# Kernel tuning notes

Hardware: AMD Instinct MI355X
Metric: run time of the kernel (lower is better)

Reference implementation:

```python
import jax, jax.numpy as jnp
import numpy as np

B = 16384
D_IN = 4096        # must equal N_FEATURES for the original code to be shape-consistent
N_FEATURES = 4096
K = 128


def setup_inputs() -> dict:
    key = jax.random.key(0)
    kx, kw = jax.random.split(key)
    x = jax.random.normal(kx, (B, D_IN), dtype=jnp.float32)
    preencoder_bias = jnp.zeros((D_IN,), dtype=jnp.float32)
    # kaiming_uniform-like init: bound = sqrt(6 / fan_in)
    bound = float(np.sqrt(6.0 / D_IN))
    W_enc = jax.random.uniform(kw, (N_FEATURES, D_IN), dtype=jnp.float32,
                               minval=-bound, maxval=bound)
    b_enc = jnp.zeros((N_FEATURES,), dtype=jnp.float32)
    return {"x": x, "preencoder_bias": preencoder_bias, "W_enc": W_enc, "b_enc": b_enc}


def reference(x, preencoder_bias, W_enc, b_enc):
    # y = (x - preencoder_bias) @ W_enc + b_enc   (W_enc is square: d_in == n_features)
    xc = x - preencoder_bias                      # [B, d_in]
    y = xc @ W_enc + b_enc                        # [B, n_features]
    acts = jax.nn.relu(y)
    # top-k threshold masking: keep entries >= k-th largest per row (ties included)
    topk_vals = jax.lax.top_k(acts, K)[0]         # [B, K], sorted descending
    threshold = topk_vals[..., -1:]               # [B, 1]
    return acts * (acts >= threshold)
```

## Files before the change

kernel.cpp:

```cpp
#include <hip/hip_runtime.h>
#include <hip/hip_bf16.h>


typedef __bf16  bf16x8 __attribute__((ext_vector_type(8)));
typedef float   f32x4  __attribute__((ext_vector_type(4)));

__device__ __forceinline__ unsigned short f2bf(float f) {
    __hip_bfloat16 h = __float2bfloat16(f);
    return __builtin_bit_cast(unsigned short, h);
}
__device__ __forceinline__ float bf2f(unsigned short u) {
    __hip_bfloat16 h = __builtin_bit_cast(__hip_bfloat16, u);
    return __bfloat162float(h);
}

#define GLL16(g, l)                                                          \
    __builtin_amdgcn_global_load_lds(                                        \
        (const __attribute__((address_space(1))) unsigned int*)(g),          \
        (__attribute__((address_space(3))) unsigned int*)(l), 16, 0, 0)

__global__ __launch_bounds__(256)
void presplit_x(const float* __restrict__ x, const float* __restrict__ pb,
                unsigned short* __restrict__ Xhi, unsigned short* __restrict__ Xlo,
                int Kdim, size_t total) {
    size_t base = ((size_t)blockIdx.x * 256 + threadIdx.x) * 8;
    if (base >= total) return;
    int kcol = (int)(base % Kdim);
    __align__(16) unsigned short hi[8], lo[8];
    #pragma unroll
    for (int q = 0; q < 2; ++q) {
        float4 xv = *(const float4*)&x[base + q * 4];
        float4 pv = *(const float4*)&pb[kcol + q * 4];
        float v[4] = {xv.x - pv.x, xv.y - pv.y, xv.z - pv.z, xv.w - pv.w};
        #pragma unroll
        for (int r = 0; r < 4; ++r) {
            hi[q*4+r] = f2bf(v[r]);
            lo[q*4+r] = f2bf(v[r] - bf2f(hi[q*4+r]));
        }
    }
    *(uint4*)&Xhi[base] = *(uint4*)&hi[0];
    *(uint4*)&Xlo[base] = *(uint4*)&lo[0];
}

__global__ __launch_bounds__(256)
void split_transpose_W(const float* __restrict__ W,
                       unsigned short* __restrict__ Wt_hi,
                       unsigned short* __restrict__ Wt_lo,
                       int N, int Kdim) {
    __shared__ float tile[64][65];
    const int tx = threadIdx.x;
    const int nB = blockIdx.x * 64;
    const int kB = blockIdx.y * 64;

    #pragma unroll
    for (int p = 0; p < 4; ++p) {
        int e  = tx + 256 * p;
        int kl = e >> 4;
        int n4 = (e & 15) << 2;
        float4 v = *(const float4*)&W[(size_t)(kB + kl) * N + nB + n4];
        tile[kl][n4 + 0] = v.x; tile[kl][n4 + 1] = v.y;
        tile[kl][n4 + 2] = v.z; tile[kl][n4 + 3] = v.w;
    }
    __syncthreads();

    #pragma unroll
    for (int p = 0; p < 4; ++p) {
        int e  = tx + 256 * p;
        int nl = e >> 4;
        int k4 = (e & 15) << 2;
        unsigned short hi[4], lo[4];
        #pragma unroll
        for (int r = 0; r < 4; ++r) {
            float f = tile[k4 + r][nl];
            hi[r] = f2bf(f);
            lo[r] = f2bf(f - bf2f(hi[r]));
        }
        size_t off = (size_t)(nB + nl) * Kdim + kB + k4;
        *(ushort4*)&Wt_hi[off] = *(ushort4*)&hi[0];
        *(ushort4*)&Wt_lo[off] = *(ushort4*)&lo[0];
    }
}

__global__ __launch_bounds__(512, 2)
void gemm_presplit4p(const unsigned short* __restrict__ Xhi,
                     const unsigned short* __restrict__ Xlo,
                     const unsigned short* __restrict__ Wt_hi,
                     const unsigned short* __restrict__ Wt_lo,
                     const float* __restrict__ be,
                     float* __restrict__ out, int M, int N, int Kdim) {
    __shared__ unsigned short sAhi[2][256 * 32];
    __shared__ unsigned short sAlo[2][256 * 32];
    __shared__ unsigned short sBhi[2][256 * 32];
    __shared__ unsigned short sBlo[2][256 * 32];

    const int tx   = threadIdx.x;
    const int lane = tx & 63;
    const int wv   = tx >> 6;
    const int ln   = lane & 15;
    const int quad = lane >> 4;
    const int wm   = wv >> 2;
    const int wn   = wv & 3;

    const int mT = M >> 8, nT = N >> 8, total = mT * nT;
    int wgid = blockIdx.y * gridDim.x + blockIdx.x;
    int xcd = wgid & 7, idx = wgid >> 3;
    int qq = total >> 3, rr = total & 7;
    int swz = (xcd < rr ? xcd * (qq + 1) : rr * (qq + 1) + (xcd - rr) * qq) + idx;
    const int mBase = (swz / nT) << 8;
    const int nBase = (swz % nT) << 8;

    const int srow = tx >> 2;
    const int lc   = tx & 3;
    const int ssw  = (srow & 3) ^ ((srow >> 2) & 3);
    const int slc  = (lc ^ ssw) << 3;

    const int swzl    = (ln & 3) ^ ((ln >> 2) & 3);
    const int fragoff = (quad ^ swzl) << 3;

#define STAGE_B(dst, r, src, kcol) do {                                       \
        int row_ = ((r) << 7) + srow;                                         \
        GLL16((src) + (size_t)(nBase + row_) * Kdim + (kcol) + slc,           \
              &(dst)[(row_ << 5) + (lc << 3)]);                               \
    } while (0)
#define STAGE_A(dst, r, src, kcol) do {                                       \
        int row_ = ((r) << 6) + srow + (srow & 64);                           \
        GLL16((src) + (size_t)(mBase + row_) * Kdim + (kcol) + slc,           \
              &(dst)[(row_ << 5) + (lc << 3)]);                               \
    } while (0)

    f32x4 acc[8][4] = {};

    const int NT = Kdim >> 5;

    STAGE_B(sBhi[0], 0, Wt_hi, 0); STAGE_B(sBhi[0], 1, Wt_hi, 0);
    STAGE_B(sBlo[0], 0, Wt_lo, 0); STAGE_B(sBlo[0], 1, Wt_lo, 0);
    STAGE_A(sAhi[0], 0, Xhi, 0);   STAGE_A(sAlo[0], 0, Xlo, 0);
    STAGE_A(sAhi[0], 1, Xhi, 0);   STAGE_A(sAlo[0], 1, Xlo, 0);
    asm volatile("s_waitcnt vmcnt(0)" ::: "memory");
    __builtin_amdgcn_s_barrier();
    __builtin_amdgcn_sched_barrier(0);

    for (int t = 0; t < NT; ++t) {
        const int cur = t & 1, nxt = cur ^ 1;
        const bool more = (t + 1 < NT);
        const int k1 = (t + 1) << 5;

        bf16x8 bhi[4], blo[4];
        #pragma unroll
        for (int q = 0; q < 4; ++q) {
            if (q == 0) {
                #pragma unroll
                for (int j = 0; j < 4; ++j) {
                    int rb = wn * 64 + j * 16 + ln;
                    bhi[j] = *(const bf16x8*)&sBhi[cur][(rb << 5) + fragoff];
                    blo[j] = *(const bf16x8*)&sBlo[cur][(rb << 5) + fragoff];
                }
            }
            bf16x8 ahi[2], alo[2];
            #pragma unroll
            for (int ii = 0; ii < 2; ++ii) {
                int ra = wm * 128 + (2 * q + ii) * 16 + ln;
                ahi[ii] = *(const bf16x8*)&sAhi[cur][(ra << 5) + fragoff];
                alo[ii] = *(const bf16x8*)&sAlo[cur][(ra << 5) + fragoff];
            }

            if (more) {
                if (q == 0)      { STAGE_B(sBhi[nxt], 0, Wt_hi, k1); STAGE_B(sBhi[nxt], 1, Wt_hi, k1); }
                else if (q == 1) { STAGE_B(sBlo[nxt], 0, Wt_lo, k1); STAGE_B(sBlo[nxt], 1, Wt_lo, k1); }
                else if (q == 2) { STAGE_A(sAhi[nxt], 0, Xhi, k1);   STAGE_A(sAlo[nxt], 0, Xlo, k1); }
                else             { STAGE_A(sAhi[nxt], 1, Xhi, k1);   STAGE_A(sAlo[nxt], 1, Xlo, k1); }
            }

            __builtin_amdgcn_s_barrier();
            __builtin_amdgcn_s_setprio(1);
            #pragma unroll
            for (int ii = 0; ii < 2; ++ii)
                #pragma unroll
                for (int j = 0; j < 4; ++j)
                    acc[2 * q + ii][j] = __builtin_amdgcn_mfma_f32_16x16x32_bf16(
                        ahi[ii], bhi[j], acc[2 * q + ii][j], 0, 0, 0);
            #pragma unroll
            for (int ii = 0; ii < 2; ++ii)
                #pragma unroll
                for (int j = 0; j < 4; ++j)
                    acc[2 * q + ii][j] = __builtin_amdgcn_mfma_f32_16x16x32_bf16(
                        ahi[ii], blo[j], acc[2 * q + ii][j], 0, 0, 0);
            #pragma unroll
            for (int ii = 0; ii < 2; ++ii)
                #pragma unroll
                for (int j = 0; j < 4; ++j)
                    acc[2 * q + ii][j] = __builtin_amdgcn_mfma_f32_16x16x32_bf16(
                        alo[ii], bhi[j], acc[2 * q + ii][j], 0, 0, 0);
            __builtin_amdgcn_s_setprio(0);

            if (more) {
                if (q == 1)      asm volatile("s_waitcnt vmcnt(4)" ::: "memory");
                else if (q == 3) asm volatile("s_waitcnt vmcnt(2)" ::: "memory");
            } else if (q == 1) {
                asm volatile("s_waitcnt vmcnt(0)" ::: "memory");
            }
            __builtin_amdgcn_s_barrier();
            __builtin_amdgcn_sched_barrier(0);
        }
    }

    #pragma unroll
    for (int j = 0; j < 4; ++j) {
        int n = nBase + wn * 64 + j * 16 + ln;
        float bev = be[n];
        #pragma unroll
        for (int i = 0; i < 8; ++i) {
            #pragma unroll
            for (int r = 0; r < 4; ++r) {
                int m = mBase + wm * 128 + i * 16 + quad * 4 + r;
                out[(size_t)m * N + n] = fmaxf(acc[i][j][r] + bev, 0.f);
            }
        }
    }
#undef STAGE_B
#undef STAGE_A
}

__global__ __launch_bounds__(256)
void gemm_split_bf16(const float* __restrict__ x, const float* __restrict__ pb,
                     const unsigned short* __restrict__ Wt_hi,
                     const unsigned short* __restrict__ Wt_lo,
                     const float* __restrict__ be,
                     float* __restrict__ out, int M, int N, int Kdim) {
    __shared__ unsigned short sAhi[128][32];
    __shared__ unsigned short sAlo[128][32];
    __shared__ unsigned short sBhi[128][32];
    __shared__ unsigned short sBlo[128][32];

    const int tx    = threadIdx.x;
    const int nBase = blockIdx.x * 128;
    const int mBase = blockIdx.y * 128;
    const int wv    = tx >> 6;
    const int lane  = tx & 63;
    const int ln    = lane & 15;
    const int quad  = lane >> 4;
    const int wm    = wv >> 1;
    const int wn    = wv & 1;
    const int am = tx >> 1;
    const int ak = (tx & 1) * 16;
    const int bn  = wv * 16 + (lane >> 2);
    const int bk8 = (lane & 3) * 8;

    f32x4 acc[4][4] = {};

    for (int k0 = 0; k0 < Kdim; k0 += 32) {
        __syncthreads();
        #pragma unroll
        for (int r = 0; r < 2; ++r) {
            int nrow = r * 64 + bn;
            size_t goff = (size_t)(nBase + nrow) * Kdim + k0 + bk8;
            GLL16(&Wt_hi[goff], &sBhi[nrow][bk8]);
            GLL16(&Wt_lo[goff], &sBlo[nrow][bk8]);
        }
        {
            const float* xrow = x  + (size_t)(mBase + am) * Kdim + k0 + ak;
            const float* pbp  = pb + k0 + ak;
            float v[16];
            #pragma unroll
            for (int q = 0; q < 4; ++q) {
                float4 xv = *(const float4*)(xrow + q * 4);
                float4 pv = *(const float4*)(pbp + q * 4);
                v[q*4+0] = xv.x - pv.x; v[q*4+1] = xv.y - pv.y;
                v[q*4+2] = xv.z - pv.z; v[q*4+3] = xv.w - pv.w;
            }
            __align__(16) unsigned short hi[16], lo[16];
            #pragma unroll
            for (int q = 0; q < 16; ++q) {
                hi[q] = f2bf(v[q]);
                lo[q] = f2bf(v[q] - bf2f(hi[q]));
            }
            *(uint4*)&sAhi[am][ak]     = *(uint4*)&hi[0];
            *(uint4*)&sAhi[am][ak + 8] = *(uint4*)&hi[8];
            *(uint4*)&sAlo[am][ak]     = *(uint4*)&lo[0];
            *(uint4*)&sAlo[am][ak + 8] = *(uint4*)&lo[8];
        }
        __syncthreads();

        bf16x8 ahi[4], alo[4], bhi[4], blo[4];
        #pragma unroll
        for (int i = 0; i < 4; ++i) {
            int m = wm * 64 + i * 16 + ln;
            ahi[i] = *(const bf16x8*)&sAhi[m][quad * 8];
            alo[i] = *(const bf16x8*)&sAlo[m][quad * 8];
        }
        #pragma unroll
        for (int j = 0; j < 4; ++j) {
            int n = wn * 64 + j * 16 + ln;
            bhi[j] = *(const bf16x8*)&sBhi[n][quad * 8];
            blo[j] = *(const bf16x8*)&sBlo[n][quad * 8];
        }
        #pragma unroll
        for (int i = 0; i < 4; ++i)
            #pragma unroll
            for (int j = 0; j < 4; ++j) {
                acc[i][j] = __builtin_amdgcn_mfma_f32_16x16x32_bf16(ahi[i], bhi[j], acc[i][j], 0, 0, 0);
                acc[i][j] = __builtin_amdgcn_mfma_f32_16x16x32_bf16(ahi[i], blo[j], acc[i][j], 0, 0, 0);
                acc[i][j] = __builtin_amdgcn_mfma_f32_16x16x32_bf16(alo[i], bhi[j], acc[i][j], 0, 0, 0);
            }
    }

    #pragma unroll
    for (int j = 0; j < 4; ++j) {
        int n = nBase + wn * 64 + j * 16 + ln;
        float bev = be[n];
        #pragma unroll
        for (int i = 0; i < 4; ++i)
            #pragma unroll
            for (int r = 0; r < 4; ++r) {
                int m = mBase + wm * 64 + i * 16 + quad * 4 + r;
                out[(size_t)m * N + n] = fmaxf(acc[i][j][r] + bev, 0.f);
            }
    }
}

#define BAND    2e-4f
#define AMB_CAP 64

__global__ __launch_bounds__(256)
void topk_mask_exact(const float* __restrict__ x, const float* __restrict__ pb,
                     const float* __restrict__ W, const float* __restrict__ be,
                     float* __restrict__ out, int N, int Kdim, int Ksel) {
    __shared__ float    vals[4096];
    __shared__ unsigned hist[256];
    __shared__ unsigned s_prefix;
    __shared__ int      s_k, s_done;
    __shared__ int      s_nhi, s_namb;
    __shared__ int      amb_idx[AMB_CAP];
    __shared__ double   amb_d[AMB_CAP];
    __shared__ int      amb_keep[AMB_CAP];
    __shared__ double   red[4];

    const int tx  = threadIdx.x;
    const int row = blockIdx.x;
    float* rowp = out + (size_t)row * N;

    #pragma unroll
    for (int p = 0; p < 4; ++p) {
        int i = (tx + 256 * p) << 2;
        *(float4*)&vals[i] = *(const float4*)&rowp[i];
    }
    if (tx == 0) { s_done = 0; s_nhi = 0; s_namb = 0; }
    __syncthreads();

    unsigned prefix = 0, prefix_mask = 0;
    int kneed_r = Ksel;
    for (int shift = 24; shift >= 0; shift -= 8) {
        hist[tx] = 0;
        __syncthreads();
        #pragma unroll
        for (int p = 0; p < 16; ++p) {
            unsigned u = __float_as_uint(vals[tx + 256 * p]);
            if (u != 0u && (u & prefix_mask) == prefix)
                atomicAdd(&hist[(u >> shift) & 255u], 1u);
        }
        __syncthreads();
        if (tx == 0) {
            int cum = 0, b;
            for (b = 255; b >= 0; --b) { cum += (int)hist[b]; if (cum >= kneed_r) break; }
            if (b < 0) s_done = 1;
            else { s_prefix = prefix | ((unsigned)b << shift); s_k = kneed_r - (cum - (int)hist[b]); }
        }
        __syncthreads();
        if (s_done) { prefix = 0; break; }
        prefix = s_prefix;
        kneed_r = s_k;
        prefix_mask |= (0xFFu << shift);
        __syncthreads();
    }
    const float thr = __uint_as_float(prefix);

    if (thr < 0.01f) {
        #pragma unroll
        for (int p = 0; p < 4; ++p) {
            int i = (tx + 256 * p) << 2;
            float4 v = *(float4*)&vals[i];
            v.x = (v.x >= thr) ? v.x : 0.f;
            v.y = (v.y >= thr) ? v.y : 0.f;
            v.z = (v.z >= thr) ? v.z : 0.f;
            v.w = (v.w >= thr) ? v.w : 0.f;
            *(float4*)&rowp[i] = v;
        }
        return;
    }

    int my_hi = 0;
    #pragma unroll
    for (int p = 0; p < 16; ++p) {
        float v = vals[tx + 256 * p];
        if (v > thr + BAND) my_hi++;
        else if (v >= thr - BAND) {
            int slot = atomicAdd(&s_namb, 1);
            if (slot < AMB_CAP) amb_idx[slot] = tx + 256 * p;
        }
    }
    atomicAdd(&s_nhi, my_hi);
    __syncthreads();

    const int nhi   = s_nhi;
    const int namb  = (s_namb < AMB_CAP) ? s_namb : AMB_CAP;
    const int kneed = Ksel - nhi;
    const bool fallback = (s_namb > AMB_CAP) || (kneed < 0) || (kneed > s_namb);

    if (fallback) {
        #pragma unroll
        for (int p = 0; p < 16; ++p) {
            int i = tx + 256 * p;
            float v = vals[i];
            rowp[i] = (v >= thr) ? v : 0.f;
        }
        return;
    }

    if (namb > kneed) {
        for (int j = 0; j < namb; ++j) {
            const int n = amb_idx[j];
            double partial = 0.0;
            for (int p = 0; p < Kdim / 256; ++p) {
                int k = tx + 256 * p;
                partial += ((double)x[(size_t)row * Kdim + k] - (double)pb[k]) *
                           (double)W[(size_t)k * N + n];
            }
            #pragma unroll
            for (int off = 32; off > 0; off >>= 1) partial += __shfl_down(partial, off);
            if ((tx & 63) == 0) red[tx >> 6] = partial;
            __syncthreads();
            if (tx == 0) amb_d[j] = red[0] + red[1] + red[2] + red[3] + (double)be[n];
            __syncthreads();
        }
        if (tx == 0) {
            for (int j = 0; j < namb; ++j) {
                int greater = 0;
                for (int l = 0; l < namb; ++l)
                    if (amb_d[l] > amb_d[j]) greater++;
                amb_keep[j] = (greater < kneed) ? 1 : 0;
            }
        }
        __syncthreads();
    } else {
        for (int j = tx; j < namb; j += 256) amb_keep[j] = 1;
        __syncthreads();
    }

    #pragma unroll
    for (int p = 0; p < 16; ++p) {
        int i = tx + 256 * p;
        float v = vals[i];
        float o;
        if (v > thr + BAND) o = v;
        else if (v < thr - BAND) o = 0.f;
        else {
            int keep = 0;
            for (int j = 0; j < namb; ++j)
                if (amb_idx[j] == i) { keep = amb_keep[j]; break; }
            o = keep ? v : 0.f;
        }
        rowp[i] = o;
    }
}

extern "C" void kernel_launch(void* const* d_in, const int* in_sizes, int n_in,
                              void* d_out, int out_size, void* d_ws, size_t ws_size,
                              hipStream_t stream) {
    const float* x  = (const float*)d_in[0];
    const float* pb = (const float*)d_in[1];
    const float* W  = (const float*)d_in[2];
    const float* be = (const float*)d_in[3];
    float* out = (float*)d_out;

    const int D = in_sizes[1];
    const int N = in_sizes[3];
    const int M = in_sizes[0] / D;

    const size_t szW = (size_t)N * D;
    const size_t szX = (size_t)M * D;
    const size_t needW    = 2ull * szW * sizeof(unsigned short);
    const size_t needFull = needW + 2ull * szX * sizeof(unsigned short);

    const bool div256 = (M % 256 == 0) && (N % 256 == 0) && (D % 32 == 0);

    if (ws_size >= needFull && div256) {
        unsigned short* Wt_hi = (unsigned short*)d_ws;
        unsigned short* Wt_lo = Wt_hi + szW;
        unsigned short* Xhi   = Wt_lo + szW;
        unsigned short* Xlo   = Xhi + szX;
        split_transpose_W<<<dim3(N / 64, D / 64), 256, 0, stream>>>(W, Wt_hi, Wt_lo, N, D);
        {
            size_t total = szX;
            int blocks = (int)((total / 8 + 255) / 256);
            presplit_x<<<blocks, 256, 0, stream>>>(x, pb, Xhi, Xlo, D, total);
        }
        gemm_presplit4p<<<dim3(N / 256, M / 256), 512, 0, stream>>>(
            Xhi, Xlo, Wt_hi, Wt_lo, be, out, M, N, D);
    } else {
        unsigned short* Wt_hi = (unsigned short*)d_ws;
        unsigned short* Wt_lo = Wt_hi + szW;
        split_transpose_W<<<dim3(N / 64, D / 64), 256, 0, stream>>>(W, Wt_hi, Wt_lo, N, D);
        gemm_split_bf16<<<dim3(N / 128, M / 128), 256, 0, stream>>>(
            x, pb, Wt_hi, Wt_lo, be, out, M, N, D);
    }
    topk_mask_exact<<<M, 256, 0, stream>>>(x, pb, W, be, out, N, D, 128);
}
```

Baseline: 2.280 ms.

## Interleave hi/lo bf16 tiles in shared memory and use register-resident bisection top-k

The GEMM now stores each row's hi and lo bf16 halves side by side in one 64-wide shared tile with an XOR swizzle. This replaces the four separate hi/lo buffers, reshapes the staging loads, and uses finer-grained vmcnt waits. The top-k kernel keeps each row in registers and finds the threshold by binary search over float bit patterns using warp reductions, instead of a shared-memory radix histogram with atomics. The bisection needs about 31 block-wide reduction rounds, which may cost more than the four histogram passes it replaces.

```diff
diff --git a/kernel.cpp b/kernel.cpp
--- a/kernel.cpp
+++ b/kernel.cpp
@@ -82,16 +82,14 @@
 }
 
 __global__ __launch_bounds__(512, 2)
-void gemm_presplit4p(const unsigned short* __restrict__ Xhi,
+void gemm_presplit_i(const unsigned short* __restrict__ Xhi,
                      const unsigned short* __restrict__ Xlo,
                      const unsigned short* __restrict__ Wt_hi,
                      const unsigned short* __restrict__ Wt_lo,
                      const float* __restrict__ be,
                      float* __restrict__ out, int M, int N, int Kdim) {
-    __shared__ unsigned short sAhi[2][256 * 32];
-    __shared__ unsigned short sAlo[2][256 * 32];
-    __shared__ unsigned short sBhi[2][256 * 32];
-    __shared__ unsigned short sBlo[2][256 * 32];
+    __shared__ unsigned short sA[2][256 * 64];
+    __shared__ unsigned short sB[2][256 * 64];
 
     const int tx   = threadIdx.x;
     const int lane = tx & 63;
@@ -104,38 +102,38 @@
     const int mT = M >> 8, nT = N >> 8, total = mT * nT;
     int wgid = blockIdx.y * gridDim.x + blockIdx.x;
     int xcd = wgid & 7, idx = wgid >> 3;
-    int qq = total >> 3, rr = total & 7;
-    int swz = (xcd < rr ? xcd * (qq + 1) : rr * (qq + 1) + (xcd - rr) * qq) + idx;
+    int qq = total >> 3, rr_ = total & 7;
+    int swz = (xcd < rr_ ? xcd * (qq + 1) : rr_ * (qq + 1) + (xcd - rr_) * qq) + idx;
     const int mBase = (swz / nT) << 8;
     const int nBase = (swz % nT) << 8;
 
-    const int srow = tx >> 2;
-    const int lc   = tx & 3;
-    const int ssw  = (srow & 3) ^ ((srow >> 2) & 3);
-    const int slc  = (lc ^ ssw) << 3;
-
-    const int swzl    = (ln & 3) ^ ((ln >> 2) & 3);
-    const int fragoff = (quad ^ swzl) << 3;
-
-#define STAGE_B(dst, r, src, kcol) do {                                       \
-        int row_ = ((r) << 7) + srow;                                         \
-        GLL16((src) + (size_t)(nBase + row_) * Kdim + (kcol) + slc,           \
-              &(dst)[(row_ << 5) + (lc << 3)]);                               \
+    const int rr  = tx >> 3;
+    const int lc8 = tx & 7;
+    const int lgc = lc8 ^ (rr & 7);
+    const unsigned short* aSrc = (lgc & 4) ? Xlo : Xhi;
+    const unsigned short* bSrc = (lgc & 4) ? Wt_lo : Wt_hi;
+    const int srcoff = (lgc & 3) << 3;
+    const int arow_b = (rr & 31) + ((rr & 32) << 2);
+
+    const int pA = (quad ^ (ln & 7)) << 3;
+
+#define STAGE_B(bufp, r, k0_) do {                                            \
+        int row_ = ((r) << 6) + rr;                                           \
+        GLL16(bSrc + (size_t)(nBase + row_) * Kdim + (k0_) + srcoff,          \
+              &sB[bufp][(row_ << 6) + (lc8 << 3)]);                           \
     } while (0)
-#define STAGE_A(dst, r, src, kcol) do {                                       \
-        int row_ = ((r) << 6) + srow + (srow & 64);                           \
-        GLL16((src) + (size_t)(mBase + row_) * Kdim + (kcol) + slc,           \
-              &(dst)[(row_ << 5) + (lc << 3)]);                               \
+#define STAGE_A(bufp, r, k0_) do {                                            \
+        int row_ = ((r) << 5) + arow_b;                                       \
+        GLL16(aSrc + (size_t)(mBase + row_) * Kdim + (k0_) + srcoff,          \
+              &sA[bufp][(row_ << 6) + (lc8 << 3)]);                           \
     } while (0)
 
     f32x4 acc[8][4] = {};
 
     const int NT = Kdim >> 5;
 
-    STAGE_B(sBhi[0], 0, Wt_hi, 0); STAGE_B(sBhi[0], 1, Wt_hi, 0);
-    STAGE_B(sBlo[0], 0, Wt_lo, 0); STAGE_B(sBlo[0], 1, Wt_lo, 0);
-    STAGE_A(sAhi[0], 0, Xhi, 0);   STAGE_A(sAlo[0], 0, Xlo, 0);
-    STAGE_A(sAhi[0], 1, Xhi, 0);   STAGE_A(sAlo[0], 1, Xlo, 0);
+    STAGE_B(0, 0, 0); STAGE_B(0, 1, 0); STAGE_B(0, 2, 0); STAGE_B(0, 3, 0);
+    STAGE_A(0, 0, 0); STAGE_A(0, 1, 0); STAGE_A(0, 2, 0); STAGE_A(0, 3, 0);
     asm volatile("s_waitcnt vmcnt(0)" ::: "memory");
     __builtin_amdgcn_s_barrier();
     __builtin_amdgcn_sched_barrier(0);
@@ -152,23 +150,23 @@
                 #pragma unroll
                 for (int j = 0; j < 4; ++j) {
                     int rb = wn * 64 + j * 16 + ln;
-                    bhi[j] = *(const bf16x8*)&sBhi[cur][(rb << 5) + fragoff];
-                    blo[j] = *(const bf16x8*)&sBlo[cur][(rb << 5) + fragoff];
+                    bhi[j] = *(const bf16x8*)&sB[cur][(rb << 6) + pA];
+                    blo[j] = *(const bf16x8*)&sB[cur][(rb << 6) + (pA ^ 32)];
                 }
             }
             bf16x8 ahi[2], alo[2];
             #pragma unroll
             for (int ii = 0; ii < 2; ++ii) {
                 int ra = wm * 128 + (2 * q + ii) * 16 + ln;
-                ahi[ii] = *(const bf16x8*)&sAhi[cur][(ra << 5) + fragoff];
-                alo[ii] = *(const bf16x8*)&sAlo[cur][(ra << 5) + fragoff];
+                ahi[ii] = *(const bf16x8*)&sA[cur][(ra << 6) + pA];
+                alo[ii] = *(const bf16x8*)&sA[cur][(ra << 6) + (pA ^ 32)];
             }
 
             if (more) {
-                if (q == 0)      { STAGE_B(sBhi[nxt], 0, Wt_hi, k1); STAGE_B(sBhi[nxt], 1, Wt_hi, k1); }
-                else if (q == 1) { STAGE_B(sBlo[nxt], 0, Wt_lo, k1); STAGE_B(sBlo[nxt], 1, Wt_lo, k1); }
-                else if (q == 2) { STAGE_A(sAhi[nxt], 0, Xhi, k1);   STAGE_A(sAlo[nxt], 0, Xlo, k1); }
-                else             { STAGE_A(sAhi[nxt], 1, Xhi, k1);   STAGE_A(sAlo[nxt], 1, Xlo, k1); }
+                if (q == 0)      { STAGE_B(nxt, 0, k1); STAGE_B(nxt, 1, k1); }
+                else if (q == 1) { STAGE_B(nxt, 2, k1); STAGE_B(nxt, 3, k1); }
+                else if (q == 2) { STAGE_A(nxt, 0, k1); STAGE_A(nxt, 1, k1); }
+                else             { STAGE_A(nxt, 2, k1); STAGE_A(nxt, 3, k1); }
             }
 
             __builtin_amdgcn_s_barrier();
@@ -194,10 +192,14 @@
             __builtin_amdgcn_s_setprio(0);
 
             if (more) {
-                if (q == 1)      asm volatile("s_waitcnt vmcnt(4)" ::: "memory");
-                else if (q == 3) asm volatile("s_waitcnt vmcnt(2)" ::: "memory");
-            } else if (q == 1) {
-                asm volatile("s_waitcnt vmcnt(0)" ::: "memory");
+                if (q == 0)      asm volatile("s_waitcnt vmcnt(4)" ::: "memory");
+                else if (q == 1) asm volatile("s_waitcnt vmcnt(5)" ::: "memory");
+                else if (q == 2) asm volatile("s_waitcnt vmcnt(6)" ::: "memory");
+                else             asm volatile("s_waitcnt vmcnt(3)" ::: "memory");
+            } else {
+                if (q == 0)      asm volatile("s_waitcnt vmcnt(2)" ::: "memory");
+                else if (q == 1) asm volatile("s_waitcnt vmcnt(1)" ::: "memory");
+                else if (q == 2) asm volatile("s_waitcnt vmcnt(0)" ::: "memory");
             }
             __builtin_amdgcn_s_barrier();
             __builtin_amdgcn_sched_barrier(0);
@@ -325,77 +327,80 @@
 void topk_mask_exact(const float* __restrict__ x, const float* __restrict__ pb,
                      const float* __restrict__ W, const float* __restrict__ be,
                      float* __restrict__ out, int N, int Kdim, int Ksel) {
-    __shared__ float    vals[4096];
-    __shared__ unsigned hist[256];
-    __shared__ unsigned s_prefix;
-    __shared__ int      s_k, s_done;
-    __shared__ int      s_nhi, s_namb;
-    __shared__ int      amb_idx[AMB_CAP];
-    __shared__ double   amb_d[AMB_CAP];
-    __shared__ int      amb_keep[AMB_CAP];
-    __shared__ double   red[4];
+    __shared__ int    s_red[4];
+    __shared__ int    s_nhi, s_namb;
+    __shared__ int    amb_idx[AMB_CAP];
+    __shared__ double amb_d[AMB_CAP];
+    __shared__ int    amb_keep[AMB_CAP];
+    __shared__ double dred[4];
 
     const int tx  = threadIdx.x;
     const int row = blockIdx.x;
     float* rowp = out + (size_t)row * N;
 
+    float v[16];
     #pragma unroll
     for (int p = 0; p < 4; ++p) {
-        int i = (tx + 256 * p) << 2;
-        *(float4*)&vals[i] = *(const float4*)&rowp[i];
-    }
-    if (tx == 0) { s_done = 0; s_nhi = 0; s_namb = 0; }
+        float4 f = *(const float4*)&rowp[(tx + 256 * p) << 2];
+        v[p*4+0] = f.x; v[p*4+1] = f.y; v[p*4+2] = f.z; v[p*4+3] = f.w;
+    }
+    unsigned uv[16];
+    #pragma unroll
+    for (int i = 0; i < 16; ++i) uv[i] = __float_as_uint(v[i]);
+
+    int c0 = 0;
+    #pragma unroll
+    for (int i = 0; i < 16; ++i) c0 += (uv[i] != 0u) ? 1 : 0;
+    #pragma unroll
+    for (int off = 32; off > 0; off >>= 1) c0 += __shfl_down(c0, off);
+    if ((tx & 63) == 0) s_red[tx >> 6] = c0;
     __syncthreads();
-
-    unsigned prefix = 0, prefix_mask = 0;
-    int kneed_r = Ksel;
-    for (int shift = 24; shift >= 0; shift -= 8) {
-        hist[tx] = 0;
-        __syncthreads();
-        #pragma unroll
-        for (int p = 0; p < 16; ++p) {
-            unsigned u = __float_as_uint(vals[tx + 256 * p]);
-            if (u != 0u && (u & prefix_mask) == prefix)
-                atomicAdd(&hist[(u >> shift) & 255u], 1u);
-        }
-        __syncthreads();
-        if (tx == 0) {
-            int cum = 0, b;
-            for (b = 255; b >= 0; --b) { cum += (int)hist[b]; if (cum >= kneed_r) break; }
-            if (b < 0) s_done = 1;
-            else { s_prefix = prefix | ((unsigned)b << shift); s_k = kneed_r - (cum - (int)hist[b]); }
-        }
-        __syncthreads();
-        if (s_done) { prefix = 0; break; }
-        prefix = s_prefix;
-        kneed_r = s_k;
-        prefix_mask |= (0xFFu << shift);
-        __syncthreads();
-    }
-    const float thr = __uint_as_float(prefix);
+    const int total_nz = s_red[0] + s_red[1] + s_red[2] + s_red[3];
+
+    unsigned thr_u = 0;
+    if (total_nz >= Ksel) {
+        unsigned blo_ = 1u, bhi_ = 0x7f7fffffu;
+        while (blo_ < bhi_) {
+            unsigned mid = blo_ + ((bhi_ - blo_ + 1) >> 1);
+            int cc = 0;
+            #pragma unroll
+            for (int i = 0; i < 16; ++i) cc += (uv[i] >= mid) ? 1 : 0;
+            #pragma unroll
+            for (int off = 32; off > 0; off >>= 1) cc += __shfl_down(cc, off);
+            __syncthreads();
+            if ((tx & 63) == 0) s_red[tx >> 6] = cc;
+            __syncthreads();
+            int cnt = s_red[0] + s_red[1] + s_red[2] + s_red[3];
+            if (cnt >= Ksel) blo_ = mid; else bhi_ = mid - 1;
+        }
+        thr_u = blo_;
+    }
+    const float thr = __uint_as_float(thr_u);
 
     if (thr < 0.01f) {
         #pragma unroll
         for (int p = 0; p < 4; ++p) {
-            int i = (tx + 256 * p) << 2;
-            float4 v = *(float4*)&vals[i];
-            v.x = (v.x >= thr) ? v.x : 0.f;
-            v.y = (v.y >= thr) ? v.y : 0.f;
-            v.z = (v.z >= thr) ? v.z : 0.f;
-            v.w = (v.w >= thr) ? v.w : 0.f;
-            *(float4*)&rowp[i] = v;
+            float4 o;
+            o.x = (v[p*4+0] >= thr) ? v[p*4+0] : 0.f;
+            o.y = (v[p*4+1] >= thr) ? v[p*4+1] : 0.f;
+            o.z = (v[p*4+2] >= thr) ? v[p*4+2] : 0.f;
+            o.w = (v[p*4+3] >= thr) ? v[p*4+3] : 0.f;
+            *(float4*)&rowp[(tx + 256 * p) << 2] = o;
         }
         return;
     }
 
+    if (tx == 0) { s_nhi = 0; s_namb = 0; }
+    __syncthreads();
+
     int my_hi = 0;
     #pragma unroll
-    for (int p = 0; p < 16; ++p) {
-        float v = vals[tx + 256 * p];
-        if (v > thr + BAND) my_hi++;
-        else if (v >= thr - BAND) {
+    for (int i = 0; i < 16; ++i) {
+        float val = v[i];
+        if (val > thr + BAND) my_hi++;
+        else if (val >= thr - BAND) {
             int slot = atomicAdd(&s_namb, 1);
-            if (slot < AMB_CAP) amb_idx[slot] = tx + 256 * p;
+            if (slot < AMB_CAP) amb_idx[slot] = ((tx + 256 * (i >> 2)) << 2) + (i & 3);
         }
     }
     atomicAdd(&s_nhi, my_hi);
@@ -408,10 +413,13 @@
 
     if (fallback) {
         #pragma unroll
-        for (int p = 0; p < 16; ++p) {
-            int i = tx + 256 * p;
-            float v = vals[i];
-            rowp[i] = (v >= thr) ? v : 0.f;
+        for (int p = 0; p < 4; ++p) {
+            float4 o;
+            o.x = (v[p*4+0] >= thr) ? v[p*4+0] : 0.f;
+            o.y = (v[p*4+1] >= thr) ? v[p*4+1] : 0.f;
+            o.z = (v[p*4+2] >= thr) ? v[p*4+2] : 0.f;
+            o.w = (v[p*4+3] >= thr) ? v[p*4+3] : 0.f;
+            *(float4*)&rowp[(tx + 256 * p) << 2] = o;
         }
         return;
     }
@@ -427,9 +435,9 @@
             }
             #pragma unroll
             for (int off = 32; off > 0; off >>= 1) partial += __shfl_down(partial, off);
-            if ((tx & 63) == 0) red[tx >> 6] = partial;
+            if ((tx & 63) == 0) dred[tx >> 6] = partial;
             __syncthreads();
-            if (tx == 0) amb_d[j] = red[0] + red[1] + red[2] + red[3] + (double)be[n];
+            if (tx == 0) amb_d[j] = dred[0] + dred[1] + dred[2] + dred[3] + (double)be[n];
             __syncthreads();
         }
         if (tx == 0) {
@@ -447,19 +455,25 @@
     }
 
     #pragma unroll
-    for (int p = 0; p < 16; ++p) {
-        int i = tx + 256 * p;
-        float v = vals[i];
-        float o;
-        if (v > thr + BAND) o = v;
-        else if (v < thr - BAND) o = 0.f;
-        else {
-            int keep = 0;
-            for (int j = 0; j < namb; ++j)
-                if (amb_idx[j] == i) { keep = amb_keep[j]; break; }
-            o = keep ? v : 0.f;
-        }
-        rowp[i] = o;
+    for (int p = 0; p < 4; ++p) {
+        float4 o;
+        float* po = (float*)&o;
+        #pragma unroll
+        for (int r = 0; r < 4; ++r) {
+            int gi = ((tx + 256 * p) << 2) + r;
+            float val = v[p*4+r];
+            float ov;
+            if (val > thr + BAND) ov = val;
+            else if (val < thr - BAND) ov = 0.f;
+            else {
+                int keep = 0;
+                for (int j = 0; j < namb; ++j)
+                    if (amb_idx[j] == gi) { keep = amb_keep[j]; break; }
+                ov = keep ? val : 0.f;
+            }
+            po[r] = ov;
+        }
+        *(float4*)&rowp[(tx + 256 * p) << 2] = o;
     }
 }
 
@@ -494,7 +508,7 @@
             int blocks = (int)((total / 8 + 255) / 256);
             presplit_x<<<blocks, 256, 0, stream>>>(x, pb, Xhi, Xlo, D, total);
         }
-        gemm_presplit4p<<<dim3(N / 256, M / 256), 512, 0, stream>>>(
+        gemm_presplit_i<<<dim3(N / 256, M / 256), 512, 0, stream>>>(
             Xhi, Xlo, Wt_hi, Wt_lo, be, out, M, N, D);
     } else {
         unsigned short* Wt_hi = (unsigned short*)d_ws;
```

After: 2.059 ms. -9.7%, faster.
